# Performance work log

Hardware: AMD Instinct MI355X
Metric: run time of the kernel (lower is better)

The kernel has to match this reference:

```python
import jax, jax.numpy as jnp
import numpy as np

N, E, F, H, EF, NC, GC, G = 50000, 800000, 128, 128, 6, 8, 4, 64
NEG_SLOPE = 0.01  # torch F.leaky_relu default
EPS = 1e-5        # torch BatchNorm1d default


def _gconv(x, W, b, src, dst):
    # DGL GraphConv, norm='both': D_dst^{-1/2} A D_src^{-1/2} X W + b (degrees clamped to >=1)
    n = x.shape[0]
    ones = jnp.ones(src.shape[0], x.dtype)
    out_deg = jnp.maximum(jax.ops.segment_sum(ones, src, num_segments=n), 1.0)
    in_deg = jnp.maximum(jax.ops.segment_sum(ones, dst, num_segments=n), 1.0)
    xs = x * jax.lax.rsqrt(out_deg)[:, None]          # [N, F] scaled by src norm
    agg = jax.ops.segment_sum(xs[src], dst, num_segments=n)  # gather->scatter-add over edges
    agg = agg * jax.lax.rsqrt(in_deg)[:, None]
    return agg @ W + b


def _bn(h, gamma, beta):
    # BatchNorm1d in training mode: batch statistics, biased variance
    mu = h.mean(0)
    var = jnp.mean((h - mu) ** 2, 0)
    return (h - mu) * jax.lax.rsqrt(var + EPS) * gamma + beta


def _lrelu(x):
    return jnp.where(x >= 0, x, NEG_SLOPE * x)


def setup_inputs() -> dict:
    ks = jax.random.split(jax.random.key(0), 24)
    def Wmat(i, shape):
        return jax.random.normal(ks[i], shape, jnp.float32) / np.float32(np.sqrt(shape[0]))
    node_feat = jax.random.normal(ks[0], (N, F), jnp.float32)
    nodetype = jax.random.uniform(ks[1], (N,), jnp.float32)
    edge_feat = jax.random.normal(ks[2], (E, EF), jnp.float32)
    src = jax.random.randint(ks[3], (E,), 0, N, jnp.int32)
    dst = jax.random.randint(ks[4], (E,), 0, N, jnp.int32)
    graph_ids = jnp.sort(jax.random.randint(ks[5], (N,), 0, G, jnp.int32))
    return {
        "node_feat": node_feat, "nodetype": nodetype, "edge_feat": edge_feat,
        "W1": Wmat(6, (F, H)), "b1": jnp.zeros(H, jnp.float32),
        "gamma1": jnp.ones(H, jnp.float32), "beta1": jnp.zeros(H, jnp.float32),
        "W2": Wmat(7, (H, H)), "b2": jnp.zeros(H, jnp.float32),
        "gamma2": jnp.ones(H, jnp.float32), "beta2": jnp.zeros(H, jnp.float32),
        "We": Wmat(8, (EF, H)), "b_e": jnp.zeros(H, jnp.float32),
        "Wn1": Wmat(9, (H, H)), "b_nn1": jnp.zeros(H, jnp.float32),
        "Wn2": Wmat(10, (H, H)), "b_nn2": jnp.zeros(H, jnp.float32),
        "Wnc": Wmat(11, (H, NC)), "b_nc": jnp.zeros(NC, jnp.float32),
        "Wg1": Wmat(12, (H + 1, H)), "b_g1": jnp.zeros(H, jnp.float32),
        "Wgc": Wmat(13, (H, GC)), "b_gc": jnp.zeros(GC, jnp.float32),
        "src": src, "dst": dst, "graph_ids": graph_ids,
    }


def reference(node_feat, nodetype, edge_feat, W1, b1, gamma1, beta1, W2, b2, gamma2, beta2,
              We, b_e, Wn1, b_nn1, Wn2, b_nn2, Wnc, b_nc, Wg1, b_g1, Wgc, b_gc,
              src, dst, graph_ids):
    h = _lrelu(_bn(_gconv(node_feat, W1, b1, src, dst), gamma1, beta1))
    h = _lrelu(_bn(_gconv(h, W2, b2, src, dst), gamma2, beta2))
    # apply_edges: m = src['h'] + linear_edge(edge_feat); stored in edata but never read (dead in original too)
    m = h[src] + edge_feat @ We + b_e  # noqa: F841
    hn = _lrelu(_gconv(h, Wn1, b_nn1, src, dst))
    hn = _lrelu(_gconv(hn, Wn2, b_nn2, src, dst))
    node_out = hn @ Wnc + b_nc                                   # [N, NC]
    hg = jnp.concatenate([h, nodetype[:, None]], axis=1)         # [N, H+1]
    hg = _lrelu(_gconv(hg, Wg1, b_g1, src, dst))
    counts = jnp.maximum(jax.ops.segment_sum(jnp.ones(N, hg.dtype), graph_ids, num_segments=G), 1.0)
    hgm = jax.ops.segment_sum(hg, graph_ids, num_segments=G) / counts[:, None]  # dgl.mean_nodes
    graph_out = hgm @ Wgc + b_gc                                 # [G, GC]
    return (node_out, graph_out)
```

## Files before the change

kernel.cpp:

```cpp
#include <hip/hip_runtime.h>
#include <cstdint>
#include <cstddef>

#define NN 50000
#define NE 800000
#define HD 128
#define GK 16
#define HNB 64

typedef __attribute__((ext_vector_type(8))) short bf16x8;
typedef __attribute__((ext_vector_type(4))) float f32x4;
typedef _Float16 f16x4 __attribute__((ext_vector_type(4)));
typedef _Float16 f16x8 __attribute__((ext_vector_type(8)));

__device__ inline unsigned short f2bf(float x) {
  unsigned u = __float_as_uint(x);
  u += 0x7FFF + ((u >> 16) & 1);
  return (unsigned short)(u >> 16);
}
__device__ inline float bf2f(unsigned short h) { return __uint_as_float((unsigned)h << 16); }

__global__ __launch_bounds__(256) void deghist_kernel(const int* __restrict__ src, const int* __restrict__ dst,
                                                      int* __restrict__ part, int e) {
  __shared__ int hist[25000];
  const int b = blockIdx.x >> 2;
  const int sel = (blockIdx.x >> 1) & 1;
  const int h = blockIdx.x & 1;
  const int* arr = sel ? dst : src;
  for (int i = threadIdx.x; i < 25000; i += 256) hist[i] = 0;
  __syncthreads();
  const int lo = h * 25000;
  const int slice = e >> 6;
  const int base = b * slice;
  for (int i = base + threadIdx.x; i < base + slice; i += 256) {
    int v = arr[i] - lo;
    if ((unsigned)v < 25000u) atomicAdd(&hist[v], 1);
  }
  __syncthreads();
  int* out = part + ((size_t)(sel * 2 + h) * HNB + b) * 25000;
  for (int i = threadIdx.x; i < 25000; i += 256) out[i] = hist[i];
}

__global__ __launch_bounds__(256) void degred_kernel(const int* __restrict__ part, int* __restrict__ incnt,
                                                     float* __restrict__ rs_out, float* __restrict__ rs_in, int n) {
  int v = blockIdx.x * 256 + threadIdx.x;
  if (v >= n) return;
  const int h = (v >= 25000) ? 1 : 0;
  const int bin = v - h * 25000;
  const int* p0 = part + ((size_t)(0 + h) * HNB) * 25000 + bin;
  const int* p1 = part + ((size_t)(2 + h) * HNB) * 25000 + bin;
  int os = 0, is = 0;
#pragma unroll 8
  for (int b = 0; b < HNB; b++) {
    os += p0[(size_t)b * 25000];
    is += p1[(size_t)b * 25000];
  }
  incnt[v] = is;
  rs_out[v] = rsqrtf((float)(os > 1 ? os : 1));
  rs_in[v] = rsqrtf((float)(is > 1 ? is : 1));
}

__global__ __launch_bounds__(256) void scan1_kernel(const int* __restrict__ cnt, int* __restrict__ excl,
                                                    int* __restrict__ bsum, int n) {
  __shared__ int sh[256];
  int i = blockIdx.x * 256 + threadIdx.x;
  int v = (i < n) ? cnt[i] : 0;
  sh[threadIdx.x] = v;
  __syncthreads();
  for (int off = 1; off < 256; off <<= 1) {
    int x = (threadIdx.x >= off) ? sh[threadIdx.x - off] : 0;
    __syncthreads();
    sh[threadIdx.x] += x;
    __syncthreads();
  }
  if (i < n) excl[i] = sh[threadIdx.x] - v;
  if (threadIdx.x == 255) bsum[blockIdx.x] = sh[255];
}

__global__ __launch_bounds__(256) void scan2_kernel(int* __restrict__ bsum, int nb) {
  __shared__ int sh[256];
  int v = (threadIdx.x < nb) ? bsum[threadIdx.x] : 0;
  sh[threadIdx.x] = v;
  __syncthreads();
  for (int off = 1; off < 256; off <<= 1) {
    int x = (threadIdx.x >= off) ? sh[threadIdx.x - off] : 0;
    __syncthreads();
    sh[threadIdx.x] += x;
    __syncthreads();
  }
  if (threadIdx.x < nb) bsum[threadIdx.x] = sh[threadIdx.x] - v;
}

__global__ __launch_bounds__(256) void scan3_kernel(const int* __restrict__ excl, const int* __restrict__ bsum,
                                                    int* __restrict__ row_ptr, int n, int e) {
  int i = blockIdx.x * 256 + threadIdx.x;
  if (i < n) row_ptr[i] = excl[i] + bsum[blockIdx.x];
  if (i == 0) row_ptr[n] = e;
}

__global__ __launch_bounds__(256) void scanoffs_kernel(const int* __restrict__ part, const int* __restrict__ row_ptr,
                                                       int* __restrict__ offs, int n) {
  int v = blockIdx.x * 256 + threadIdx.x;
  if (v >= n) return;
  const int h = (v >= 25000) ? 1 : 0;
  const int bin = v - h * 25000;
  const int* p = part + ((size_t)(2 + h) * HNB) * 25000 + bin;
  int run = row_ptr[v];
#pragma unroll 8
  for (int b = 0; b < HNB; b++) {
    offs[((size_t)(b * 2 + h)) * 25000 + bin] = run;
    run += p[(size_t)b * 25000];
  }
}

__global__ __launch_bounds__(256) void fill2_kernel(const int* __restrict__ src, const int* __restrict__ dst,
                                                    const int* __restrict__ offs, int* __restrict__ csr_src, int e) {
  __shared__ int cur[25000];
  const int b = blockIdx.x >> 1;
  const int h = blockIdx.x & 1;
  const int* o = offs + ((size_t)(b * 2 + h)) * 25000;
  for (int i = threadIdx.x; i < 25000; i += 256) cur[i] = o[i];
  __syncthreads();
  const int lo = h * 25000;
  const int slice = e >> 6;
  const int base = b * slice;
  for (int i = base + threadIdx.x; i < base + slice; i += 256) {
    int v = dst[i] - lo;
    if ((unsigned)v < 25000u) {
      int pos = atomicAdd(&cur[v], 1);
      csr_src[pos] = src[i];
    }
  }
}

__global__ __launch_bounds__(256) void convw_kernel(const float* __restrict__ W1, const float* __restrict__ W2,
                                                    const float* __restrict__ Wn1, const float* __restrict__ Wn2,
                                                    const float* __restrict__ Wg1, unsigned short* __restrict__ Wp) {
  const float* Ws[5] = {W1, W2, Wn1, Wn2, Wg1};
  const float* W = Ws[blockIdx.x];
  unsigned short* hi = Wp + (size_t)blockIdx.x * 32768;
  unsigned short* lo = hi + 16384;
  for (int s = threadIdx.x; s < 2048; s += 256) {
    int f = s >> 6, lane = s & 63;
    int ct = f >> 2, ks = f & 3;
    int col = ct * 16 + (lane & 15);
    int k0 = ks * 32 + ((lane >> 4) << 3);
    for (int j = 0; j < 8; j++) {
      float v = W[(k0 + j) * HD + col];
      unsigned short h = f2bf(v);
      hi[s * 8 + j] = h;
      lo[s * 8 + j] = f2bf(v - bf2f(h));
    }
  }
}

template <int MODE>
__global__ __launch_bounds__(256) void mmfma_kernel(const void* __restrict__ Ain,
                                                    const float* __restrict__ bnp,
                                                    const unsigned short* __restrict__ Wp,
                                                    const float* __restrict__ rs,
                                                    const float* __restrict__ evec,
                                                    const float* __restrict__ erow,
                                                    _Float16* __restrict__ C, int n) {
  const int lane = threadIdx.x & 63;
  const int wv = threadIdx.x >> 6;
  const int rbase = (blockIdx.x * 4 + wv) * 16;
  if (rbase >= n) return;
  const int rA = min(rbase + (lane & 15), n - 1);
  const int koff = (lane >> 4) << 3;
  const unsigned short* wlo = Wp + 16384;
  f32x4 acc[8];
#pragma unroll
  for (int t = 0; t < 8; t++) acc[t] = (f32x4){0.f, 0.f, 0.f, 0.f};
#pragma unroll
  for (int ks = 0; ks < 4; ks++) {
    const int c0 = ks * 32 + koff;
    float av[8];
    if (MODE == 0) {
      const float* ap = (const float*)Ain + (size_t)rA * HD + c0;
      float4 a0 = *reinterpret_cast<const float4*>(ap);
      float4 a1 = *reinterpret_cast<const float4*>(ap + 4);
      av[0] = a0.x; av[1] = a0.y; av[2] = a0.z; av[3] = a0.w;
      av[4] = a1.x; av[5] = a1.y; av[6] = a1.z; av[7] = a1.w;
    } else {
      const _Float16* ap = (const _Float16*)Ain + (size_t)rA * HD + c0;
      f16x8 a = *reinterpret_cast<const f16x8*>(ap);
#pragma unroll
      for (int j = 0; j < 8; j++) av[j] = (float)a[j];
    }
    if (MODE == 1) {
      float4 s0 = *reinterpret_cast<const float4*>(bnp + c0);
      float4 s1 = *reinterpret_cast<const float4*>(bnp + c0 + 4);
      float4 t0 = *reinterpret_cast<const float4*>(bnp + 128 + c0);
      float4 t1 = *reinterpret_cast<const float4*>(bnp + 128 + c0 + 4);
      float sc[8] = {s0.x, s0.y, s0.z, s0.w, s1.x, s1.y, s1.z, s1.w};
      float sf[8] = {t0.x, t0.y, t0.z, t0.w, t1.x, t1.y, t1.z, t1.w};
#pragma unroll
      for (int j = 0; j < 8; j++) {
        float x = fmaf(av[j], sc[j], sf[j]);
        av[j] = x >= 0.f ? x : 0.01f * x;
      }
    }
    bf16x8 ah, al;
#pragma unroll
    for (int j = 0; j < 8; j++) {
      unsigned short hh = f2bf(av[j]);
      ((short*)&ah)[j] = (short)hh;
      ((short*)&al)[j] = (short)f2bf(av[j] - bf2f(hh));
    }
#pragma unroll
    for (int ct = 0; ct < 8; ct++) {
      int fo = ((ct * 4 + ks) * 64 + lane) * 8;
      bf16x8 bh = *reinterpret_cast<const bf16x8*>(Wp + fo);
      bf16x8 bl = *reinterpret_cast<const bf16x8*>(wlo + fo);
      acc[ct] = __builtin_amdgcn_mfma_f32_16x16x32_bf16(ah, bh, acc[ct], 0, 0, 0);
      acc[ct] = __builtin_amdgcn_mfma_f32_16x16x32_bf16(al, bh, acc[ct], 0, 0, 0);
      acc[ct] = __builtin_amdgcn_mfma_f32_16x16x32_bf16(ah, bl, acc[ct], 0, 0, 0);
    }
  }
  const int r0 = rbase + ((lane >> 4) << 2);
  const int cbase = lane & 15;
#pragma unroll
  for (int i = 0; i < 4; i++) {
    int r = r0 + i;
    if (r < n) {
      float rsv = rs[r];
      float ev = (evec != nullptr) ? evec[r] : 0.f;
      _Float16* crow = C + (size_t)r * HD + cbase;
#pragma unroll
      for (int ct = 0; ct < 8; ct++) {
        float v = acc[ct][i];
        if (evec != nullptr) v = fmaf(ev, erow[ct * 16 + cbase], v);
        crow[ct * 16] = (_Float16)(v * rsv);
      }
    }
  }
}

__global__ __launch_bounds__(256) void agg_kernel(const _Float16* __restrict__ Ys, const int* __restrict__ row_ptr,
                                                  const int* __restrict__ csr_src, const float* __restrict__ rs_in,
                                                  const float* __restrict__ bias, _Float16* __restrict__ out,
                                                  int n, int do_lrelu) {
  const int wave = threadIdx.x >> 6;
  const int lane = threadIdx.x & 63;
  const int half = lane >> 5;
  const int li = lane & 31;
  const int node = blockIdx.x * 4 + wave;
  if (node >= n) return;
  const int beg = row_ptr[node], end = row_ptr[node + 1];
  const int cnt = end - beg;
  const int npairs = cnt >> 1;
  float a0 = 0.f, a1 = 0.f, a2 = 0.f, a3 = 0.f;
  int p = 0;
  for (; p + 8 <= npairs; p += 8) {
    int s[8];
#pragma unroll
    for (int j = 0; j < 8; j++) s[j] = csr_src[beg + 2 * (p + j) + half];
    f16x4 v[8];
#pragma unroll
    for (int j = 0; j < 8; j++) v[j] = reinterpret_cast<const f16x4*>(Ys + (size_t)s[j] * HD)[li];
#pragma unroll
    for (int j = 0; j < 8; j++) {
      a0 += (float)v[j].x;
      a1 += (float)v[j].y;
      a2 += (float)v[j].z;
      a3 += (float)v[j].w;
    }
  }
  for (; p < npairs; ++p) {
    int s = csr_src[beg + 2 * p + half];
    f16x4 v = reinterpret_cast<const f16x4*>(Ys + (size_t)s * HD)[li];
    a0 += (float)v.x;
    a1 += (float)v.y;
    a2 += (float)v.z;
    a3 += (float)v.w;
  }
  if ((cnt & 1) && half == 0) {
    int s = csr_src[end - 1];
    f16x4 v = reinterpret_cast<const f16x4*>(Ys + (size_t)s * HD)[li];
    a0 += (float)v.x;
    a1 += (float)v.y;
    a2 += (float)v.z;
    a3 += (float)v.w;
  }
  a0 += __shfl_xor(a0, 32, 64);
  a1 += __shfl_xor(a1, 32, 64);
  a2 += __shfl_xor(a2, 32, 64);
  a3 += __shfl_xor(a3, 32, 64);
  if (half == 0) {
    float ri = rs_in[node];
    float4 b = reinterpret_cast<const float4*>(bias)[li];
    float o0 = fmaf(a0, ri, b.x);
    float o1 = fmaf(a1, ri, b.y);
    float o2 = fmaf(a2, ri, b.z);
    float o3 = fmaf(a3, ri, b.w);
    if (do_lrelu) {
      o0 = o0 >= 0.f ? o0 : 0.01f * o0;
      o1 = o1 >= 0.f ? o1 : 0.01f * o1;
      o2 = o2 >= 0.f ? o2 : 0.01f * o2;
      o3 = o3 >= 0.f ? o3 : 0.01f * o3;
    }
    f16x4 ov = {(_Float16)o0, (_Float16)o1, (_Float16)o2, (_Float16)o3};
    reinterpret_cast<f16x4*>(out + (size_t)node * HD)[li] = ov;
  }
}

__global__ __launch_bounds__(256) void stats_kernel(const _Float16* __restrict__ Z, int n, float* __restrict__ sums) {
  int c = threadIdx.x & 127;
  int half = threadIdx.x >> 7;
  float s = 0.f, s2 = 0.f;
  for (int r = blockIdx.x * 2 + half; r < n; r += gridDim.x * 2) {
    float v = (float)Z[(size_t)r * HD + c];
    s += v;
    s2 = fmaf(v, v, s2);
  }
  __shared__ float ls[512];
  ls[threadIdx.x] = s;
  ls[256 + threadIdx.x] = s2;
  __syncthreads();
  if (threadIdx.x < 128) {
    atomicAdd(&sums[c], ls[threadIdx.x] + ls[threadIdx.x + 128]);
    atomicAdd(&sums[128 + c], ls[256 + threadIdx.x] + ls[256 + threadIdx.x + 128]);
  }
}

__global__ void bnfin_kernel(const float* __restrict__ sums, const float* __restrict__ gamma,
                             const float* __restrict__ beta, float* __restrict__ bnp, float n) {
  int c = threadIdx.x;
  float mu = sums[c] / n;
  float var = sums[128 + c] / n - mu * mu;
  if (var < 0.f) var = 0.f;
  float sc = gamma[c] * rsqrtf(var + 1e-5f);
  bnp[c] = sc;
  bnp[128 + c] = fmaf(-mu, sc, beta[c]);
}

__global__ __launch_bounds__(256) void nodeout_kernel(const _Float16* __restrict__ X, const float* __restrict__ Wnc,
                                                      const float* __restrict__ b, float* __restrict__ out, int n) {
  __shared__ float Wl[HD * 8];
  __shared__ float bl[8];
  for (int i = threadIdx.x; i < HD * 8; i += 256) Wl[i] = Wnc[i];
  if (threadIdx.x < 8) bl[threadIdx.x] = b[threadIdx.x];
  __syncthreads();
  int t = blockIdx.x * 256 + threadIdx.x;
  int r = t >> 3, c = t & 7;
  if (r >= n) return;
  const _Float16* x = X + (size_t)r * HD;
  float acc = bl[c];
  for (int k = 0; k < HD; k += 4) {
    f16x4 a = *reinterpret_cast<const f16x4*>(x + k);
    acc = fmaf((float)a.x, Wl[k * 8 + c], acc);
    acc = fmaf((float)a.y, Wl[(k + 1) * 8 + c], acc);
    acc = fmaf((float)a.z, Wl[(k + 2) * 8 + c], acc);
    acc = fmaf((float)a.w, Wl[(k + 3) * 8 + c], acc);
  }
  out[(size_t)r * 8 + c] = acc;
}

__global__ __launch_bounds__(256) void gpart_kernel(const _Float16* __restrict__ HG, const int* __restrict__ gid,
                                                    float* __restrict__ partial, int n) {
  const int g = blockIdx.x >> 4;
  const int j = blockIdx.x & 15;
  int lo = 0, hi = n;
  while (lo < hi) { int mid = (lo + hi) >> 1; if (gid[mid] < g) lo = mid + 1; else hi = mid; }
  const int beg = lo;
  lo = 0; hi = n;
  while (lo < hi) { int mid = (lo + hi) >> 1; if (gid[mid] < g + 1) lo = mid + 1; else hi = mid; }
  const int end = lo;
  const int len = end - beg;
  const int chunk = (len + GK - 1) / GK;
  const int r0 = beg + j * chunk;
  const int r1 = min(r0 + chunk, end);

  const int c = threadIdx.x & 127;
  const int half = threadIdx.x >> 7;
  float s = 0.f;
  for (int r = r0 + half; r < r1; r += 2)
    s += (float)HG[(size_t)r * HD + c];

  __shared__ float sh[256];
  sh[threadIdx.x] = s;
  __syncthreads();
  if (threadIdx.x < 128)
    partial[(size_t)blockIdx.x * HD + threadIdx.x] = sh[threadIdx.x] + sh[threadIdx.x + 128];
}

__global__ __launch_bounds__(128) void gfin_kernel(const float* __restrict__ partial, const int* __restrict__ gid,
                                                   const float* __restrict__ Wgc, const float* __restrict__ bgc,
                                                   float* __restrict__ out, int n) {
  const int g = blockIdx.x;
  int lo = 0, hi = n;
  while (lo < hi) { int mid = (lo + hi) >> 1; if (gid[mid] < g) lo = mid + 1; else hi = mid; }
  const int beg = lo;
  lo = 0; hi = n;
  while (lo < hi) { int mid = (lo + hi) >> 1; if (gid[mid] < g + 1) lo = mid + 1; else hi = mid; }
  const int end = lo;
  float cntf = (float)(end - beg);
  float inv = 1.f / (cntf > 1.f ? cntf : 1.f);

  const int c = threadIdx.x;
  float s = 0.f;
#pragma unroll
  for (int j = 0; j < GK; j++) s += partial[(size_t)(g * GK + j) * HD + c];
  __shared__ float sh[128];
  sh[c] = s * inv;
  __syncthreads();
  if (c < 4) {
    float acc = bgc[c];
    for (int k = 0; k < HD; k++) acc = fmaf(sh[k], Wgc[k * 4 + c], acc);
    out[g * 4 + c] = acc;
  }
}

extern "C" void kernel_launch(void* const* d_in, const int* in_sizes, int n_in,
                              void* d_out, int out_size, void* d_ws, size_t ws_size,
                              hipStream_t stream) {
  const float* node_feat = (const float*)d_in[0];
  const float* nodetype = (const float*)d_in[1];
  const float* W1 = (const float*)d_in[3];
  const float* b1 = (const float*)d_in[4];
  const float* g1 = (const float*)d_in[5];
  const float* be1 = (const float*)d_in[6];
  const float* W2 = (const float*)d_in[7];
  const float* b2 = (const float*)d_in[8];
  const float* g2 = (const float*)d_in[9];
  const float* be2 = (const float*)d_in[10];
  const float* Wn1 = (const float*)d_in[13];
  const float* bn1 = (const float*)d_in[14];
  const float* Wn2 = (const float*)d_in[15];
  const float* bn2 = (const float*)d_in[16];
  const float* Wnc = (const float*)d_in[17];
  const float* bnc = (const float*)d_in[18];
  const float* Wg1 = (const float*)d_in[19];
  const float* bg1 = (const float*)d_in[20];
  const float* Wgc = (const float*)d_in[21];
  const float* bgc = (const float*)d_in[22];
  const int* src = (const int*)d_in[23];
  const int* dst = (const int*)d_in[24];
  const int* gid = (const int*)d_in[25];

  const int n = NN, e = NE;

  char* w = (char*)d_ws;
  auto alloc = [&](size_t bytes) -> void* {
    void* p = (void*)w;
    w += (bytes + 255) & ~(size_t)255;
    return p;
  };
  _Float16* T1 = (_Float16*)alloc((size_t)n * HD * 4);
  _Float16* AX = (_Float16*)alloc((size_t)n * HD * 2);
  _Float16* A2 = (_Float16*)alloc((size_t)n * HD * 2);
  int* hpart = (int*)T1;
  int* offs = (int*)A2;
  int* csr_src = (int*)alloc((size_t)e * 4);
  int* row_ptr = (int*)alloc((size_t)(n + 1) * 4);
  int* incnt = (int*)alloc((size_t)n * 4);
  int* excl = (int*)alloc((size_t)n * 4);
  int* bsum = (int*)alloc(256 * 4);
  float* rs_out = (float*)alloc((size_t)n * 4);
  float* rs_in = (float*)alloc((size_t)n * 4);
  float* sums = (float*)alloc(256 * 4);
  float* bnp1 = (float*)alloc(256 * 4);
  float* bnp2 = (float*)alloc(256 * 4);
  unsigned short* Wp = (unsigned short*)alloc(5 * 32768 * 2);
  float* partial = (float*)alloc((size_t)64 * GK * HD * 4);

  const int NB = (n + 255) / 256;
  const int MMB = (n + 63) / 64;
  const int AGB = (n + 3) / 4;
  const int NOB = (n * 8 + 255) / 256;

  convw_kernel<<<5, 256, 0, stream>>>(W1, W2, Wn1, Wn2, Wg1, Wp);

  deghist_kernel<<<HNB * 4, 256, 0, stream>>>(src, dst, hpart, e);
  degred_kernel<<<NB, 256, 0, stream>>>(hpart, incnt, rs_out, rs_in, n);
  scan1_kernel<<<NB, 256, 0, stream>>>(incnt, excl, bsum, n);
  scan2_kernel<<<1, 256, 0, stream>>>(bsum, NB);
  scan3_kernel<<<NB, 256, 0, stream>>>(excl, bsum, row_ptr, n, e);
  scanoffs_kernel<<<NB, 256, 0, stream>>>(hpart, row_ptr, offs, n);
  fill2_kernel<<<HNB * 2, 256, 0, stream>>>(src, dst, offs, csr_src, e);

  mmfma_kernel<0><<<MMB, 256, 0, stream>>>(node_feat, nullptr, Wp + 0 * 32768, rs_out, nullptr, nullptr, T1, n);
  agg_kernel<<<AGB, 256, 0, stream>>>(T1, row_ptr, csr_src, rs_in, b1, AX, n, 0);
  hipMemsetAsync(sums, 0, 256 * 4, stream);
  stats_kernel<<<256, 256, 0, stream>>>(AX, n, sums);
  bnfin_kernel<<<1, 128, 0, stream>>>(sums, g1, be1, bnp1, (float)n);

  mmfma_kernel<1><<<MMB, 256, 0, stream>>>(AX, bnp1, Wp + 1 * 32768, rs_out, nullptr, nullptr, T1, n);
  agg_kernel<<<AGB, 256, 0, stream>>>(T1, row_ptr, csr_src, rs_in, b2, A2, n, 0);
  hipMemsetAsync(sums, 0, 256 * 4, stream);
  stats_kernel<<<256, 256, 0, stream>>>(A2, n, sums);
  bnfin_kernel<<<1, 128, 0, stream>>>(sums, g2, be2, bnp2, (float)n);

  mmfma_kernel<1><<<MMB, 256, 0, stream>>>(A2, bnp2, Wp + 2 * 32768, rs_out, nullptr, nullptr, T1, n);
  agg_kernel<<<AGB, 256, 0, stream>>>(T1, row_ptr, csr_src, rs_in, bn1, AX, n, 1);

  mmfma_kernel<2><<<MMB, 256, 0, stream>>>(AX, nullptr, Wp + 3 * 32768, rs_out, nullptr, nullptr, T1, n);
  agg_kernel<<<AGB, 256, 0, stream>>>(T1, row_ptr, csr_src, rs_in, bn2, AX, n, 1);

  nodeout_kernel<<<NOB, 256, 0, stream>>>(AX, Wnc, bnc, (float*)d_out, n);

  mmfma_kernel<1><<<MMB, 256, 0, stream>>>(A2, bnp2, Wp + 4 * 32768, rs_out, nodetype, Wg1 + HD * HD, T1, n);
  agg_kernel<<<AGB, 256, 0, stream>>>(T1, row_ptr, csr_src, rs_in, bg1, AX, n, 1);

  gpart_kernel<<<64 * GK, 256, 0, stream>>>(AX, gid, partial, n);
  gfin_kernel<<<64, 128, 0, stream>>>(partial, gid, Wgc, bgc, (float*)d_out + (size_t)n * 8, n);
}
```

Baseline: 462.8 us.

## Fuse degree reduce with scan, node-out head into aggregation, widen MFMA tiles

Merges the degree reduction and first scan pass into one kernel and drops the separate block-sum scan, with scan3 summing prior block totals serially. The node classifier projection is folded into the final aggregation kernel through a shuffle reduction, so the hidden activations are never written and the nodeout kernel is removed. BatchNorm statistics now go to per-block partial buffers reduced in bnfin, replacing atomics and the memset. Each wave in the MFMA GEMM now handles 32 rows instead of 16, reusing weight fragments across two row tiles. Together these cut launch count and global traffic, at the cost of more registers in the GEMM and a serial loop in scan3.

New measurement: 527.0 us. +13.9%, slower.

```diff
diff --git a/kernel.cpp b/kernel.cpp
--- a/kernel.cpp
+++ b/kernel.cpp
@@ -7,6 +7,7 @@
 #define HD 128
 #define GK 16
 #define HNB 64
+#define SB 128
 
 typedef __attribute__((ext_vector_type(8))) short bf16x8;
 typedef __attribute__((ext_vector_type(4))) float f32x4;
@@ -41,31 +42,27 @@
   for (int i = threadIdx.x; i < 25000; i += 256) out[i] = hist[i];
 }
 
-__global__ __launch_bounds__(256) void degred_kernel(const int* __restrict__ part, int* __restrict__ incnt,
-                                                     float* __restrict__ rs_out, float* __restrict__ rs_in, int n) {
+__global__ __launch_bounds__(256) void degscan_kernel(const int* __restrict__ part, int* __restrict__ excl,
+                                                      int* __restrict__ bsum, float* __restrict__ rs_out,
+                                                      float* __restrict__ rs_in, int n) {
   int v = blockIdx.x * 256 + threadIdx.x;
-  if (v >= n) return;
-  const int h = (v >= 25000) ? 1 : 0;
-  const int bin = v - h * 25000;
-  const int* p0 = part + ((size_t)(0 + h) * HNB) * 25000 + bin;
-  const int* p1 = part + ((size_t)(2 + h) * HNB) * 25000 + bin;
-  int os = 0, is = 0;
+  int is = 0;
+  if (v < n) {
+    const int h = (v >= 25000) ? 1 : 0;
+    const int bin = v - h * 25000;
+    const int* p0 = part + ((size_t)(0 + h) * HNB) * 25000 + bin;
+    const int* p1 = part + ((size_t)(2 + h) * HNB) * 25000 + bin;
+    int os = 0;
 #pragma unroll 8
-  for (int b = 0; b < HNB; b++) {
-    os += p0[(size_t)b * 25000];
-    is += p1[(size_t)b * 25000];
-  }
-  incnt[v] = is;
-  rs_out[v] = rsqrtf((float)(os > 1 ? os : 1));
-  rs_in[v] = rsqrtf((float)(is > 1 ? is : 1));
-}
-
-__global__ __launch_bounds__(256) void scan1_kernel(const int* __restrict__ cnt, int* __restrict__ excl,
-                                                    int* __restrict__ bsum, int n) {
+    for (int b = 0; b < HNB; b++) {
+      os += p0[(size_t)b * 25000];
+      is += p1[(size_t)b * 25000];
+    }
+    rs_out[v] = rsqrtf((float)(os > 1 ? os : 1));
+    rs_in[v] = rsqrtf((float)(is > 1 ? is : 1));
+  }
   __shared__ int sh[256];
-  int i = blockIdx.x * 256 + threadIdx.x;
-  int v = (i < n) ? cnt[i] : 0;
-  sh[threadIdx.x] = v;
+  sh[threadIdx.x] = is;
   __syncthreads();
   for (int off = 1; off < 256; off <<= 1) {
     int x = (threadIdx.x >= off) ? sh[threadIdx.x - off] : 0;
@@ -73,28 +70,16 @@
     sh[threadIdx.x] += x;
     __syncthreads();
   }
-  if (i < n) excl[i] = sh[threadIdx.x] - v;
+  if (v < n) excl[v] = sh[threadIdx.x] - is;
   if (threadIdx.x == 255) bsum[blockIdx.x] = sh[255];
-}
-
-__global__ __launch_bounds__(256) void scan2_kernel(int* __restrict__ bsum, int nb) {
-  __shared__ int sh[256];
-  int v = (threadIdx.x < nb) ? bsum[threadIdx.x] : 0;
-  sh[threadIdx.x] = v;
-  __syncthreads();
-  for (int off = 1; off < 256; off <<= 1) {
-    int x = (threadIdx.x >= off) ? sh[threadIdx.x - off] : 0;
-    __syncthreads();
-    sh[threadIdx.x] += x;
-    __syncthreads();
-  }
-  if (threadIdx.x < nb) bsum[threadIdx.x] = sh[threadIdx.x] - v;
 }
 
 __global__ __launch_bounds__(256) void scan3_kernel(const int* __restrict__ excl, const int* __restrict__ bsum,
                                                     int* __restrict__ row_ptr, int n, int e) {
+  int base = 0;
+  for (int b = 0; b < blockIdx.x; b++) base += bsum[b];
   int i = blockIdx.x * 256 + threadIdx.x;
-  if (i < n) row_ptr[i] = excl[i] + bsum[blockIdx.x];
+  if (i < n) row_ptr[i] = excl[i] + base;
   if (i == 0) row_ptr[n] = e;
 }
 
@@ -155,6 +140,37 @@
 }
 
 template <int MODE>
+__device__ inline void load_frag(const void* __restrict__ Ain, const float* __restrict__ bnp,
+                                 int rA, int c0, bf16x8& ah, bf16x8& al) {
+  float av[8];
+  if (MODE == 0) {
+    const float* ap = (const float*)Ain + (size_t)rA * HD + c0;
+    float4 a0 = *reinterpret_cast<const float4*>(ap);
+    float4 a1 = *reinterpret_cast<const float4*>(ap + 4);
+    av[0] = a0.x; av[1] = a0.y; av[2] = a0.z; av[3] = a0.w;
+    av[4] = a1.x; av[5] = a1.y; av[6] = a1.z; av[7] = a1.w;
+  } else {
+    const _Float16* ap = (const _Float16*)Ain + (size_t)rA * HD + c0;
+    f16x8 a = *reinterpret_cast<const f16x8*>(ap);
+#pragma unroll
+    for (int j = 0; j < 8; j++) av[j] = (float)a[j];
+  }
+  if (MODE == 1) {
+#pragma unroll
+    for (int j = 0; j < 8; j++) {
+      float x = fmaf(av[j], bnp[c0 + j], bnp[128 + c0 + j]);
+      av[j] = x >= 0.f ? x : 0.01f * x;
+    }
+  }
+#pragma unroll
+  for (int j = 0; j < 8; j++) {
+    unsigned short hh = f2bf(av[j]);
+    ((short*)&ah)[j] = (short)hh;
+    ((short*)&al)[j] = (short)f2bf(av[j] - bf2f(hh));
+  }
+}
+
+template <int MODE>
 __global__ __launch_bounds__(256) void mmfma_kernel(const void* __restrict__ Ain,
                                                     const float* __restrict__ bnp,
                                                     const unsigned short* __restrict__ Wp,
@@ -164,83 +180,66 @@
                                                     _Float16* __restrict__ C, int n) {
   const int lane = threadIdx.x & 63;
   const int wv = threadIdx.x >> 6;
-  const int rbase = (blockIdx.x * 4 + wv) * 16;
+  const int rbase = (blockIdx.x * 4 + wv) * 32;
   if (rbase >= n) return;
-  const int rA = min(rbase + (lane & 15), n - 1);
+  const int rA0 = min(rbase + (lane & 15), n - 1);
+  const int rA1 = min(rbase + 16 + (lane & 15), n - 1);
   const int koff = (lane >> 4) << 3;
   const unsigned short* wlo = Wp + 16384;
-  f32x4 acc[8];
-#pragma unroll
-  for (int t = 0; t < 8; t++) acc[t] = (f32x4){0.f, 0.f, 0.f, 0.f};
+  f32x4 acc0[8], acc1[8];
+#pragma unroll
+  for (int t = 0; t < 8; t++) {
+    acc0[t] = (f32x4){0.f, 0.f, 0.f, 0.f};
+    acc1[t] = (f32x4){0.f, 0.f, 0.f, 0.f};
+  }
 #pragma unroll
   for (int ks = 0; ks < 4; ks++) {
     const int c0 = ks * 32 + koff;
-    float av[8];
-    if (MODE == 0) {
-      const float* ap = (const float*)Ain + (size_t)rA * HD + c0;
-      float4 a0 = *reinterpret_cast<const float4*>(ap);
-      float4 a1 = *reinterpret_cast<const float4*>(ap + 4);
-      av[0] = a0.x; av[1] = a0.y; av[2] = a0.z; av[3] = a0.w;
-      av[4] = a1.x; av[5] = a1.y; av[6] = a1.z; av[7] = a1.w;
-    } else {
-      const _Float16* ap = (const _Float16*)Ain + (size_t)rA * HD + c0;
-      f16x8 a = *reinterpret_cast<const f16x8*>(ap);
-#pragma unroll
-      for (int j = 0; j < 8; j++) av[j] = (float)a[j];
-    }
-    if (MODE == 1) {
-      float4 s0 = *reinterpret_cast<const float4*>(bnp + c0);
-      float4 s1 = *reinterpret_cast<const float4*>(bnp + c0 + 4);
-      float4 t0 = *reinterpret_cast<const float4*>(bnp + 128 + c0);
-      float4 t1 = *reinterpret_cast<const float4*>(bnp + 128 + c0 + 4);
-      float sc[8] = {s0.x, s0.y, s0.z, s0.w, s1.x, s1.y, s1.z, s1.w};
-      float sf[8] = {t0.x, t0.y, t0.z, t0.w, t1.x, t1.y, t1.z, t1.w};
-#pragma unroll
-      for (int j = 0; j < 8; j++) {
-        float x = fmaf(av[j], sc[j], sf[j]);
-        av[j] = x >= 0.f ? x : 0.01f * x;
-      }
-    }
-    bf16x8 ah, al;
-#pragma unroll
-    for (int j = 0; j < 8; j++) {
-      unsigned short hh = f2bf(av[j]);
-      ((short*)&ah)[j] = (short)hh;
-      ((short*)&al)[j] = (short)f2bf(av[j] - bf2f(hh));
-    }
+    bf16x8 ah0, al0, ah1, al1;
+    load_frag<MODE>(Ain, bnp, rA0, c0, ah0, al0);
+    load_frag<MODE>(Ain, bnp, rA1, c0, ah1, al1);
 #pragma unroll
     for (int ct = 0; ct < 8; ct++) {
       int fo = ((ct * 4 + ks) * 64 + lane) * 8;
       bf16x8 bh = *reinterpret_cast<const bf16x8*>(Wp + fo);
       bf16x8 bl = *reinterpret_cast<const bf16x8*>(wlo + fo);
-      acc[ct] = __builtin_amdgcn_mfma_f32_16x16x32_bf16(ah, bh, acc[ct], 0, 0, 0);
-      acc[ct] = __builtin_amdgcn_mfma_f32_16x16x32_bf16(al, bh, acc[ct], 0, 0, 0);
-      acc[ct] = __builtin_amdgcn_mfma_f32_16x16x32_bf16(ah, bl, acc[ct], 0, 0, 0);
-    }
-  }
-  const int r0 = rbase + ((lane >> 4) << 2);
+      acc0[ct] = __builtin_amdgcn_mfma_f32_16x16x32_bf16(ah0, bh, acc0[ct], 0, 0, 0);
+      acc0[ct] = __builtin_amdgcn_mfma_f32_16x16x32_bf16(al0, bh, acc0[ct], 0, 0, 0);
+      acc0[ct] = __builtin_amdgcn_mfma_f32_16x16x32_bf16(ah0, bl, acc0[ct], 0, 0, 0);
+      acc1[ct] = __builtin_amdgcn_mfma_f32_16x16x32_bf16(ah1, bh, acc1[ct], 0, 0, 0);
+      acc1[ct] = __builtin_amdgcn_mfma_f32_16x16x32_bf16(al1, bh, acc1[ct], 0, 0, 0);
+      acc1[ct] = __builtin_amdgcn_mfma_f32_16x16x32_bf16(ah1, bl, acc1[ct], 0, 0, 0);
+    }
+  }
   const int cbase = lane & 15;
-#pragma unroll
-  for (int i = 0; i < 4; i++) {
-    int r = r0 + i;
-    if (r < n) {
-      float rsv = rs[r];
-      float ev = (evec != nullptr) ? evec[r] : 0.f;
-      _Float16* crow = C + (size_t)r * HD + cbase;
-#pragma unroll
-      for (int ct = 0; ct < 8; ct++) {
-        float v = acc[ct][i];
-        if (evec != nullptr) v = fmaf(ev, erow[ct * 16 + cbase], v);
-        crow[ct * 16] = (_Float16)(v * rsv);
-      }
-    }
-  }
-}
-
+#define EPI(ACC, TOFF)                                                          \
+  {                                                                             \
+    const int r0 = rbase + (TOFF) + ((lane >> 4) << 2);                         \
+    _Pragma("unroll") for (int i = 0; i < 4; i++) {                             \
+      int r = r0 + i;                                                           \
+      if (r < n) {                                                              \
+        float rsv = rs[r];                                                      \
+        float ev = (evec != nullptr) ? evec[r] : 0.f;                           \
+        _Float16* crow = C + (size_t)r * HD + cbase;                            \
+        _Pragma("unroll") for (int ct = 0; ct < 8; ct++) {                      \
+          float v = ACC[ct][i];                                                 \
+          if (evec != nullptr) v = fmaf(ev, erow[ct * 16 + cbase], v);          \
+          crow[ct * 16] = (_Float16)(v * rsv);                                  \
+        }                                                                       \
+      }                                                                         \
+    }                                                                           \
+  }
+  EPI(acc0, 0)
+  EPI(acc1, 16)
+#undef EPI
+}
+
+template <int TAIL>
 __global__ __launch_bounds__(256) void agg_kernel(const _Float16* __restrict__ Ys, const int* __restrict__ row_ptr,
                                                   const int* __restrict__ csr_src, const float* __restrict__ rs_in,
                                                   const float* __restrict__ bias, _Float16* __restrict__ out,
-                                                  int n, int do_lrelu) {
+                                                  const float* __restrict__ Wnc, const float* __restrict__ bnc,
+                                                  float* __restrict__ nout, int n, int do_lrelu) {
   const int wave = threadIdx.x >> 6;
   const int lane = threadIdx.x & 63;
   const int half = lane >> 5;
@@ -300,16 +299,49 @@
       o2 = o2 >= 0.f ? o2 : 0.01f * o2;
       o3 = o3 >= 0.f ? o3 : 0.01f * o3;
     }
-    f16x4 ov = {(_Float16)o0, (_Float16)o1, (_Float16)o2, (_Float16)o3};
-    reinterpret_cast<f16x4*>(out + (size_t)node * HD)[li] = ov;
-  }
-}
-
-__global__ __launch_bounds__(256) void stats_kernel(const _Float16* __restrict__ Z, int n, float* __restrict__ sums) {
+    if (TAIL == 0) {
+      f16x4 ov = {(_Float16)o0, (_Float16)o1, (_Float16)o2, (_Float16)o3};
+      reinterpret_cast<f16x4*>(out + (size_t)node * HD)[li] = ov;
+    } else {
+      float pr[8];
+#pragma unroll
+      for (int c = 0; c < 8; c++) pr[c] = 0.f;
+      float ov[4] = {o0, o1, o2, o3};
+#pragma unroll
+      for (int j = 0; j < 4; j++) {
+        const float* wr = Wnc + (size_t)(4 * li + j) * 8;
+        float4 w0 = *reinterpret_cast<const float4*>(wr);
+        float4 w1 = *reinterpret_cast<const float4*>(wr + 4);
+        pr[0] = fmaf(ov[j], w0.x, pr[0]);
+        pr[1] = fmaf(ov[j], w0.y, pr[1]);
+        pr[2] = fmaf(ov[j], w0.z, pr[2]);
+        pr[3] = fmaf(ov[j], w0.w, pr[3]);
+        pr[4] = fmaf(ov[j], w1.x, pr[4]);
+        pr[5] = fmaf(ov[j], w1.y, pr[5]);
+        pr[6] = fmaf(ov[j], w1.z, pr[6]);
+        pr[7] = fmaf(ov[j], w1.w, pr[7]);
+      }
+#pragma unroll
+      for (int m = 16; m >= 1; m >>= 1) {
+#pragma unroll
+        for (int c = 0; c < 8; c++) pr[c] += __shfl_xor(pr[c], m, 64);
+      }
+      if (li == 0) {
+        float4 r0 = make_float4(pr[0] + bnc[0], pr[1] + bnc[1], pr[2] + bnc[2], pr[3] + bnc[3]);
+        float4 r1 = make_float4(pr[4] + bnc[4], pr[5] + bnc[5], pr[6] + bnc[6], pr[7] + bnc[7]);
+        reinterpret_cast<float4*>(nout + (size_t)node * 8)[0] = r0;
+        reinterpret_cast<float4*>(nout + (size_t)node * 8)[1] = r1;
+      }
+    }
+  }
+}
+
+__global__ __launch_bounds__(256) void stats_kernel(const _Float16* __restrict__ Z, int n,
+                                                    float* __restrict__ pstats) {
   int c = threadIdx.x & 127;
   int half = threadIdx.x >> 7;
   float s = 0.f, s2 = 0.f;
-  for (int r = blockIdx.x * 2 + half; r < n; r += gridDim.x * 2) {
+  for (int r = blockIdx.x * 2 + half; r < n; r += SB * 2) {
     float v = (float)Z[(size_t)r * HD + c];
     s += v;
     s2 = fmaf(v, v, s2);
@@ -319,42 +351,25 @@
   ls[256 + threadIdx.x] = s2;
   __syncthreads();
   if (threadIdx.x < 128) {
-    atomicAdd(&sums[c], ls[threadIdx.x] + ls[threadIdx.x + 128]);
-    atomicAdd(&sums[128 + c], ls[256 + threadIdx.x] + ls[256 + threadIdx.x + 128]);
-  }
-}
-
-__global__ void bnfin_kernel(const float* __restrict__ sums, const float* __restrict__ gamma,
+    pstats[(size_t)blockIdx.x * 256 + threadIdx.x] = ls[threadIdx.x] + ls[threadIdx.x + 128];
+    pstats[(size_t)blockIdx.x * 256 + 128 + threadIdx.x] = ls[256 + threadIdx.x] + ls[384 + threadIdx.x];
+  }
+}
+
+__global__ void bnfin_kernel(const float* __restrict__ pstats, const float* __restrict__ gamma,
                              const float* __restrict__ beta, float* __restrict__ bnp, float n) {
   int c = threadIdx.x;
-  float mu = sums[c] / n;
-  float var = sums[128 + c] / n - mu * mu;
+  float s = 0.f, s2 = 0.f;
+  for (int j = 0; j < SB; j++) {
+    s += pstats[(size_t)j * 256 + c];
+    s2 += pstats[(size_t)j * 256 + 128 + c];
+  }
+  float mu = s / n;
+  float var = s2 / n - mu * mu;
   if (var < 0.f) var = 0.f;
   float sc = gamma[c] * rsqrtf(var + 1e-5f);
   bnp[c] = sc;
   bnp[128 + c] = fmaf(-mu, sc, beta[c]);
-}
-
-__global__ __launch_bounds__(256) void nodeout_kernel(const _Float16* __restrict__ X, const float* __restrict__ Wnc,
-                                                      const float* __restrict__ b, float* __restrict__ out, int n) {
-  __shared__ float Wl[HD * 8];
-  __shared__ float bl[8];
-  for (int i = threadIdx.x; i < HD * 8; i += 256) Wl[i] = Wnc[i];
-  if (threadIdx.x < 8) bl[threadIdx.x] = b[threadIdx.x];
-  __syncthreads();
-  int t = blockIdx.x * 256 + threadIdx.x;
-  int r = t >> 3, c = t & 7;
-  if (r >= n) return;
-  const _Float16* x = X + (size_t)r * HD;
-  float acc = bl[c];
-  for (int k = 0; k < HD; k += 4) {
-    f16x4 a = *reinterpret_cast<const f16x4*>(x + k);
-    acc = fmaf((float)a.x, Wl[k * 8 + c], acc);
-    acc = fmaf((float)a.y, Wl[(k + 1) * 8 + c], acc);
-    acc = fmaf((float)a.z, Wl[(k + 2) * 8 + c], acc);
-    acc = fmaf((float)a.w, Wl[(k + 3) * 8 + c], acc);
-  }
-  out[(size_t)r * 8 + c] = acc;
 }
 
 __global__ __launch_bounds__(256) void gpart_kernel(const _Float16* __restrict__ HG, const int* __restrict__ gid,
@@ -454,54 +469,46 @@
   int* offs = (int*)A2;
   int* csr_src = (int*)alloc((size_t)e * 4);
   int* row_ptr = (int*)alloc((size_t)(n + 1) * 4);
-  int* incnt = (int*)alloc((size_t)n * 4);
   int* excl = (int*)alloc((size_t)n * 4);
   int* bsum = (int*)alloc(256 * 4);
   float* rs_out = (float*)alloc((size_t)n * 4);
   float* rs_in = (float*)alloc((size_t)n * 4);
-  float* sums = (float*)alloc(256 * 4);
+  float* pstats = (float*)alloc((size_t)SB * 256 * 4);
   float* bnp1 = (float*)alloc(256 * 4);
   float* bnp2 = (float*)alloc(256 * 4);
   unsigned short* Wp = (unsigned short*)alloc(5 * 32768 * 2);
   float* partial = (float*)alloc((size_t)64 * GK * HD * 4);
 
   const int NB = (n + 255) / 256;
-  const int MMB = (n + 63) / 64;
+  const int MMB = (n + 127) / 128;
   const int AGB = (n + 3) / 4;
-  const int NOB = (n * 8 + 255) / 256;
 
   convw_kernel<<<5, 256, 0, stream>>>(W1, W2, Wn1, Wn2, Wg1, Wp);
 
   deghist_kernel<<<HNB * 4, 256, 0, stream>>>(src, dst, hpart, e);
-  degred_kernel<<<NB, 256, 0, stream>>>(hpart, incnt, rs_out, rs_in, n);
-  scan1_kernel<<<NB, 256, 0, stream>>>(incnt, excl, bsum, n);
-  scan2_kernel<<<1, 256, 0, stream>>>(bsum, NB);
+  degscan_kernel<<<NB, 256, 0, stream>>>(hpart, excl, bsum, rs_out, rs_in, n);
   scan3_kernel<<<NB, 256, 0, stream>>>(excl, bsum, row_ptr, n, e);
   scanoffs_kernel<<<NB, 256, 0, stream>>>(hpart, row_ptr, offs, n);
   fill2_kernel<<<HNB * 2, 256, 0, stream>>>(src, dst, offs, csr_src, e);
 
   mmfma_kernel<0><<<MMB, 256, 0, stream>>>(node_feat, nullptr, Wp + 0 * 32768, rs_out, nullptr, nullptr, T1, n);
-  agg_kernel<<<AGB, 256, 0, stream>>>(T1, row_ptr, csr_src, rs_in, b1, AX, n, 0);
-  hipMemsetAsync(sums, 0, 256 * 4, stream);
-  stats_kernel<<<256, 256, 0, stream>>>(AX, n, sums);
-  bnfin_kernel<<<1, 128, 0, stream>>>(sums, g1, be1, bnp1, (float)n);
+  agg_kernel<0><<<AGB, 256, 0, stream>>>(T1, row_ptr, csr_src, rs_in, b1, AX, nullptr, nullptr, nullptr, n, 0);
+  stats_kernel<<<SB, 256, 0, stream>>>(AX, n, pstats);
+  bnfin_kernel<<<1, 128, 0, stream>>>(pstats, g1, be1, bnp1, (float)n);
 
   mmfma_kernel<1><<<MMB, 256, 0, stream>>>(AX, bnp1, Wp + 1 * 32768, rs_out, nullptr, nullptr, T1, n);
-  agg_kernel<<<AGB, 256, 0, stream>>>(T1, row_ptr, csr_src, rs_in, b2, A2, n, 0);
-  hipMemsetAsync(sums, 0, 256 * 4, stream);
-  stats_kernel<<<256, 256, 0, stream>>>(A2, n, sums);
-  bnfin_kernel<<<1, 128, 0, stream>>>(sums, g2, be2, bnp2, (float)n);
+  agg_kernel<0><<<AGB, 256, 0, stream>>>(T1, row_ptr, csr_src, rs_in, b2, A2, nullptr, nullptr, nullptr, n, 0);
+  stats_kernel<<<SB, 256, 0, stream>>>(A2, n, pstats);
+  bnfin_kernel<<<1, 128, 0, stream>>>(pstats, g2, be2, bnp2, (float)n);
 
   mmfma_kernel<1><<<MMB, 256, 0, stream>>>(A2, bnp2, Wp + 2 * 32768, rs_out, nullptr, nullptr, T1, n);
-  agg_kernel<<<AGB, 256, 0, stream>>>(T1, row_ptr, csr_src, rs_in, bn1, AX, n, 1);
+  agg_kernel<0><<<AGB, 256, 0, stream>>>(T1, row_ptr, csr_src, rs_in, bn1, AX, nullptr, nullptr, nullptr, n, 1);
 
   mmfma_kernel<2><<<MMB, 256, 0, stream>>>(AX, nullptr, Wp + 3 * 32768, rs_out, nullptr, nullptr, T1, n);
-  agg_kernel<<<AGB, 256, 0, stream>>>(T1, row_ptr, csr_src, rs_in, bn2, AX, n, 1);
-
-  nodeout_kernel<<<NOB, 256, 0, stream>>>(AX, Wnc, bnc, (float*)d_out, n);
+  agg_kernel<1><<<AGB, 256, 0, stream>>>(T1, row_ptr, csr_src, rs_in, bn2, nullptr, Wnc, bnc, (float*)d_out, n, 1);
 
   mmfma_kernel<1><<<MMB, 256, 0, stream>>>(A2, bnp2, Wp + 4 * 32768, rs_out, nodetype, Wg1 + HD * HD, T1, n);
-  agg_kernel<<<AGB, 256, 0, stream>>>(T1, row_ptr, csr_src, rs_in, bg1, AX, n, 1);
+  agg_kernel<0><<<AGB, 256, 0, stream>>>(T1, row_ptr, csr_src, rs_in, bg1, AX, nullptr, nullptr, nullptr, n, 1);
 
   gpart_kernel<<<64 * GK, 256, 0, stream>>>(AX, gid, partial, n);
   gfin_kernel<<<64, 128, 0, stream>>>(partial, gid, Wgc, bgc, (float*)d_out + (size_t)n * 8, n);
```
